# Optimization experiments

Measured on AMD Instinct MI355X. Metric: run time of the kernel, lower is better.

## Reference

```python
import jax, jax.numpy as jnp
import numpy as np

N_SRC0, N_DST0 = 100000, 20000   # block0: 100k src -> 20k dst
N_DST1 = 4096                    # block1: 20k src -> 4096 dst (seed nodes)


def setup_inputs() -> dict:
    key = jax.random.key(0)
    ks = jax.random.split(key, 8)
    E0, E1 = 640000, 131072
    return {
        "features": jax.random.normal(ks[0], (N_SRC0, 256), jnp.float32),
        "W1": jax.random.normal(ks[1], (256, 256), jnp.float32) * (1.0 / np.sqrt(256)),
        "b1": jnp.zeros((256,), jnp.float32),
        "W2": jax.random.normal(ks[2], (256, 128), jnp.float32) * (1.0 / np.sqrt(256)),
        "b2": jnp.zeros((128,), jnp.float32),
        "src0": jax.random.randint(ks[3], (E0,), 0, N_SRC0, jnp.int32),
        "dst0": jax.random.randint(ks[4], (E0,), 0, N_DST0, jnp.int32),
        "src1": jax.random.randint(ks[5], (E1,), 0, N_DST0, jnp.int32),
        "dst1": jax.random.randint(ks[6], (E1,), 0, N_DST1, jnp.int32),
    }


def _graph_conv(src, dst, n_dst, feat, W, b):
    # DGL GraphConv, norm='both': D_out^{-1/2} gather-sum D_in^{-1/2}, then WX+b.
    n_src = feat.shape[0]
    ones = jnp.ones(src.shape[0], feat.dtype)
    out_deg = jax.ops.segment_sum(ones, src, num_segments=n_src)
    norm_src = jnp.clip(out_deg, 1.0, None) ** -0.5          # [n_src]
    h = feat * norm_src[:, None]
    agg = jax.ops.segment_sum(h[src], dst, num_segments=n_dst)  # sparse SpMM
    in_deg = jax.ops.segment_sum(ones, dst, num_segments=n_dst)
    norm_dst = jnp.clip(in_deg, 1.0, None) ** -0.5           # [n_dst]
    return (agg * norm_dst[:, None]) @ W + b


def reference(features, W1, b1, W2, b2, src0, dst0, src1, dst1):
    x = jax.nn.relu(_graph_conv(src0, dst0, N_DST0, features, W1, b1))
    x = _graph_conv(src1, dst1, N_DST1, x, W2, b2)
    return x
```

## Files before the change

kernel.cpp:

```cpp
#include <hip/hip_runtime.h>
#include <hip/hip_bf16.h>

#define K_DIM 256
#define RSTRIDE 128
#define EPB 8192

#define G0_DB 625
#define G0_SB 256
#define G0_SW 392
#define G0_DCAP 48
#define G0_SCAP 80
#define G1_DB 128
#define G1_SB 64
#define G1_SW 313
#define G1_DCAP 128
#define G1_SCAP 224

typedef short bf16x8 __attribute__((ext_vector_type(8)));
typedef float f32x4 __attribute__((ext_vector_type(4)));

static __device__ __forceinline__ unsigned short f2bf(float x) {
    __hip_bfloat16 b = __float2bfloat16(x);
    return *reinterpret_cast<unsigned short*>(&b);
}
static __device__ __forceinline__ float bflo(unsigned int p) {
    return __uint_as_float(p << 16);
}
static __device__ __forceinline__ float bfhi(unsigned int p) {
    return __uint_as_float(p & 0xffff0000u);
}

template <int NDB, int NSB, int SW, int DCAP, int SCP>
static __device__ __forceinline__ void split_graph_sp(
        const int* __restrict__ src, const int* __restrict__ dst, int E, int chunk,
        int* __restrict__ gdcnt, int* __restrict__ gscnt,
        unsigned int* __restrict__ bdst, unsigned int* __restrict__ bsrc,
        int* sh) {
    const int tid = threadIdx.x;
    const int e0 = chunk * EPB;
    const int n = min(EPB, E - e0);
    for (int i = tid; i < NDB + NSB; i += 256) sh[i] = 0;
    __syncthreads();
    for (int j = tid; j < n; j += 256) {
        int d = dst[e0 + j];
        int s = src[e0 + j];
        int bD = d >> 5;
        int rD = atomicAdd(&sh[bD], 1);
        if (rD < DCAP) bdst[((size_t)chunk * NDB + bD) * DCAP + rD] =
            ((unsigned)s << 5) | (unsigned)(d & 31);
        int bS = (int)((unsigned)s / SW);
        int rS = atomicAdd(&sh[NDB + bS], 1);
        if (rS < SCP) bsrc[((size_t)chunk * NSB + bS) * SCP + rS] = (unsigned)s;
    }
    __syncthreads();
    for (int i = tid; i < NDB; i += 256) gdcnt[chunk * NDB + i] = min(sh[i], DCAP);
    for (int i = tid; i < NSB; i += 256) gscnt[chunk * NSB + i] = min(sh[NDB + i], SCP);
}

__global__ __launch_bounds__(256) void split_mega_kernel(
        const int* __restrict__ src0, const int* __restrict__ dst0, int E0,
        const int* __restrict__ src1, const int* __restrict__ dst1, int E1,
        int* __restrict__ gdcnt0, int* __restrict__ gscnt0,
        unsigned int* __restrict__ bdst0, unsigned int* __restrict__ bsrc0,
        int* __restrict__ gdcnt1, int* __restrict__ gscnt1,
        unsigned int* __restrict__ bdst1, unsigned int* __restrict__ bsrc1,
        int nA0, int nA1,
        const float* __restrict__ feat, unsigned short* __restrict__ h, int total_f,
        int castBlocks,
        const float* __restrict__ W1, uint4* __restrict__ pw1,
        const float* __restrict__ W2, uint4* __restrict__ pw2) {
    __shared__ int sh[G0_DB + G0_SB];
    const int b = blockIdx.x;
    if (b < nA0) {
        split_graph_sp<G0_DB, G0_SB, G0_SW, G0_DCAP, G0_SCAP>(
            src0, dst0, E0, b, gdcnt0, gscnt0, bdst0, bsrc0, sh);
    } else if (b < nA0 + nA1) {
        split_graph_sp<G1_DB, G1_SB, G1_SW, G1_DCAP, G1_SCAP>(
            src1, dst1, E1, b - nA0, gdcnt1, gscnt1, bdst1, bsrc1, sh);
    } else if (b < nA0 + nA1 + castBlocks) {
        int idx = ((b - nA0 - nA1) * blockDim.x + threadIdx.x) * 8;
        if (idx >= total_f) return;
        const float4 v0 = *reinterpret_cast<const float4*>(feat + idx);
        const float4 v1 = *reinterpret_cast<const float4*>(feat + idx + 4);
        union { ushort4 u4[2]; uint4 u; } o;
        o.u4[0].x = f2bf(v0.x); o.u4[0].y = f2bf(v0.y);
        o.u4[0].z = f2bf(v0.z); o.u4[0].w = f2bf(v0.w);
        o.u4[1].x = f2bf(v1.x); o.u4[1].y = f2bf(v1.y);
        o.u4[1].z = f2bf(v1.z); o.u4[1].w = f2bf(v1.w);
        *reinterpret_cast<uint4*>(h + idx) = o.u;
    } else if (b < nA0 + nA1 + castBlocks + 32) {
        int idx = (b - nA0 - nA1 - castBlocks) * blockDim.x + threadIdx.x;
        int lane = idx & 63;
        int kt = (idx >> 6) & 7;
        int nt = idx >> 9;
        int n = nt * 16 + (lane & 15);
        int k = kt * 32 + (lane >> 4) * 8;
        union { unsigned short us[8]; uint4 u; } o;
#pragma unroll
        for (int j = 0; j < 8; ++j) o.us[j] = f2bf(W1[(size_t)(k + j) * 256 + n]);
        pw1[idx] = o.u;
    } else {
        int idx = (b - nA0 - nA1 - castBlocks - 32) * blockDim.x + threadIdx.x;
        int lane = idx & 63;
        int kt = (idx >> 6) & 7;
        int nt = idx >> 9;
        int n = nt * 16 + (lane & 15);
        int k = kt * 32 + (lane >> 4) * 8;
        union { unsigned short us[8]; uint4 u; } o;
#pragma unroll
        for (int j = 0; j < 8; ++j) o.us[j] = f2bf(W2[(size_t)(k + j) * 128 + n]);
        pw2[idx] = o.u;
    }
}

__global__ __launch_bounds__(256) void finalize_kernel(
        int nA0, int nA1,
        const unsigned int* __restrict__ bdst0, const int* __restrict__ gdcnt0,
        int* __restrict__ cnt0, int* __restrict__ esrc0,
        const unsigned int* __restrict__ bdst1, const int* __restrict__ gdcnt1,
        int* __restrict__ cnt1, int* __restrict__ esrc1,
        const unsigned int* __restrict__ bsrc0, const int* __restrict__ gscnt0,
        int* __restrict__ od0,
        const unsigned int* __restrict__ bsrc1, const int* __restrict__ gscnt1,
        int* __restrict__ od1) {
    __shared__ int sh[G0_SW];
    const int tid = threadIdx.x;
    int b = blockIdx.x;
    if (b < G0_DB + G1_DB) {
        const bool g0 = b < G0_DB;
        if (!g0) b -= G0_DB;
        const unsigned int* __restrict__ bd = g0 ? bdst0 : bdst1;
        const int* __restrict__ gc = g0 ? gdcnt0 : gdcnt1;
        const int NDB = g0 ? G0_DB : G1_DB;
        const int DCAP = g0 ? G0_DCAP : G1_DCAP;
        const int nblk = g0 ? nA0 : nA1;
        int* __restrict__ esrc = g0 ? esrc0 : esrc1;
        int* __restrict__ cnt = g0 ? cnt0 : cnt1;
        if (tid < 32) sh[tid] = 0;
        __syncthreads();
        for (int rr = (tid >> 2); rr < nblk; rr += 64) {
            const int c = gc[rr * NDB + b];
            const unsigned int* __restrict__ seg = bd + ((size_t)rr * NDB + b) * DCAP;
            for (int j = (tid & 3); j < c; j += 4) {
                unsigned v = seg[j];
                int dloc = v & 31;
                int s = (int)(v >> 5);
                int slot = atomicAdd(&sh[dloc], 1);
                if (slot < RSTRIDE) esrc[((size_t)(b * 32 + dloc) << 7) + slot] = s;
            }
        }
        __syncthreads();
        if (tid < 32) cnt[b * 32 + tid] = sh[tid];
    } else {
        b -= G0_DB + G1_DB;
        const bool g0 = b < G0_SB;
        if (!g0) b -= G0_SB;
        const unsigned int* __restrict__ bs = g0 ? bsrc0 : bsrc1;
        const int* __restrict__ gc = g0 ? gscnt0 : gscnt1;
        const int NSB = g0 ? G0_SB : G1_SB;
        const int SCP = g0 ? G0_SCAP : G1_SCAP;
        const int SW = g0 ? G0_SW : G1_SW;
        const int NN = g0 ? 100000 : 20000;
        const int nblk = g0 ? nA0 : nA1;
        int* __restrict__ od = g0 ? od0 : od1;
        for (int i = tid; i < SW; i += 256) sh[i] = 0;
        __syncthreads();
        const int base = b * SW;
        for (int rr = (tid >> 2); rr < nblk; rr += 64) {
            const int c = gc[rr * NSB + b];
            const unsigned int* __restrict__ seg = bs + ((size_t)rr * NSB + b) * SCP;
            for (int j = (tid & 3); j < c; j += 4)
                atomicAdd(&sh[(int)seg[j] - base], 1);
        }
        __syncthreads();
        for (int i = tid; i < SW; i += 256) {
            int node = base + i;
            if (node < NN) od[node] = sh[i];
        }
    }
}

template <bool NORM>
static __device__ __forceinline__ void gather4_to_lds(
        const unsigned short* __restrict__ hfeat, const int* __restrict__ esrc,
        const int* __restrict__ cnt, const int* __restrict__ od,
        int m0, int w, int lane, unsigned short (*Alds)[264]) {
#pragma unroll
    for (int k = 0; k < 4; ++k) {
        const int rloc = w * 4 + k;
        const int row = m0 + rloc;
        const int c = cnt[row];
        const int cend = min(c, RSTRIDE);
        const int* __restrict__ ep = esrc + ((size_t)row << 7);
        float a0 = 0.f, a1 = 0.f, a2 = 0.f, a3 = 0.f;
        int i = 0;
        for (; i + 3 < cend; i += 4) {
            int s0 = ep[i];
            int s1 = ep[i + 1];
            int s2 = ep[i + 2];
            int s3 = ep[i + 3];
            float n0 = NORM ? rsqrtf((float)max(od[s0], 1)) : 1.0f;
            float n1 = NORM ? rsqrtf((float)max(od[s1], 1)) : 1.0f;
            float n2 = NORM ? rsqrtf((float)max(od[s2], 1)) : 1.0f;
            float n3 = NORM ? rsqrtf((float)max(od[s3], 1)) : 1.0f;
            const uint2 p0 = *reinterpret_cast<const uint2*>(hfeat + (((size_t)s0) << 8) + lane * 4);
            const uint2 p1 = *reinterpret_cast<const uint2*>(hfeat + (((size_t)s1) << 8) + lane * 4);
            const uint2 p2 = *reinterpret_cast<const uint2*>(hfeat + (((size_t)s2) << 8) + lane * 4);
            const uint2 p3 = *reinterpret_cast<const uint2*>(hfeat + (((size_t)s3) << 8) + lane * 4);
            if (NORM) {
                a0 = fmaf(bflo(p0.x), n0, a0); a1 = fmaf(bfhi(p0.x), n0, a1);
                a2 = fmaf(bflo(p0.y), n0, a2); a3 = fmaf(bfhi(p0.y), n0, a3);
                a0 = fmaf(bflo(p1.x), n1, a0); a1 = fmaf(bfhi(p1.x), n1, a1);
                a2 = fmaf(bflo(p1.y), n1, a2); a3 = fmaf(bfhi(p1.y), n1, a3);
                a0 = fmaf(bflo(p2.x), n2, a0); a1 = fmaf(bfhi(p2.x), n2, a1);
                a2 = fmaf(bflo(p2.y), n2, a2); a3 = fmaf(bfhi(p2.y), n2, a3);
                a0 = fmaf(bflo(p3.x), n3, a0); a1 = fmaf(bfhi(p3.x), n3, a1);
                a2 = fmaf(bflo(p3.y), n3, a2); a3 = fmaf(bfhi(p3.y), n3, a3);
            } else {
                a0 += (bflo(p0.x) + bflo(p1.x)) + (bflo(p2.x) + bflo(p3.x));
                a1 += (bfhi(p0.x) + bfhi(p1.x)) + (bfhi(p2.x) + bfhi(p3.x));
                a2 += (bflo(p0.y) + bflo(p1.y)) + (bflo(p2.y) + bflo(p3.y));
                a3 += (bfhi(p0.y) + bfhi(p1.y)) + (bfhi(p2.y) + bfhi(p3.y));
            }
        }
        for (; i < cend; ++i) {
            int s0 = ep[i];
            float n0 = NORM ? rsqrtf((float)max(od[s0], 1)) : 1.0f;
            const uint2 p0 = *reinterpret_cast<const uint2*>(hfeat + (((size_t)s0) << 8) + lane * 4);
            if (NORM) {
                a0 = fmaf(bflo(p0.x), n0, a0); a1 = fmaf(bfhi(p0.x), n0, a1);
                a2 = fmaf(bflo(p0.y), n0, a2); a3 = fmaf(bfhi(p0.y), n0, a3);
            } else {
                a0 += bflo(p0.x);
                a1 += bfhi(p0.x);
                a2 += bflo(p0.y);
                a3 += bfhi(p0.y);
            }
        }
        float nd = rsqrtf((float)max(c, 1));
        ushort4 o;
        o.x = f2bf(a0 * nd);
        o.y = f2bf(a1 * nd);
        o.z = f2bf(a2 * nd);
        o.w = f2bf(a3 * nd);
        *reinterpret_cast<ushort4*>(&Alds[rloc][lane * 4]) = o;
    }
}

__global__ __launch_bounds__(256) void fused0_kernel(
        const unsigned short* __restrict__ hfeat, const int* __restrict__ esrc,
        const int* __restrict__ cnt, const int* __restrict__ od0,
        const uint4* __restrict__ pW, const float* __restrict__ bias,
        const int* __restrict__ od1, unsigned short* __restrict__ out) {
    __shared__ unsigned short Alds[16][264];
    const int m0 = blockIdx.x * 16;
    const int w = threadIdx.x >> 6;
    const int lane = threadIdx.x & 63;
    gather4_to_lds<true>(hfeat, esrc, cnt, od0, m0, w, lane, Alds);
    __syncthreads();

    bf16x8 a[8];
    const unsigned short* ap = &Alds[lane & 15][(lane >> 4) * 8];
#pragma unroll
    for (int kt = 0; kt < 8; ++kt)
        a[kt] = *reinterpret_cast<const bf16x8*>(ap + kt * 32);

    const int rbase = m0 + (lane >> 4) * 4;
    float nsv[4];
#pragma unroll
    for (int r = 0; r < 4; ++r) nsv[r] = rsqrtf((float)max(od1[rbase + r], 1));

#pragma unroll
    for (int nt = 0; nt < 4; ++nt) {
        const int n0 = w * 64 + nt * 16;
        f32x4 acc = {0.f, 0.f, 0.f, 0.f};
#pragma unroll
        for (int kt = 0; kt < 8; ++kt) {
            bf16x8 b = *reinterpret_cast<const bf16x8*>(&pW[((size_t)(n0 >> 4) * 8 + kt) * 64 + lane]);
            acc = __builtin_amdgcn_mfma_f32_16x16x32_bf16(a[kt], b, acc, 0, 0, 0);
        }
        const int col = n0 + (lane & 15);
        const float bv = bias[col];
#pragma unroll
        for (int r = 0; r < 4; ++r) {
            float v = fmaxf(acc[r] + bv, 0.0f) * nsv[r];
            out[(size_t)(rbase + r) * K_DIM + col] = f2bf(v);
        }
    }
}

__global__ __launch_bounds__(256) void fused1_kernel(
        const unsigned short* __restrict__ xb, const int* __restrict__ esrc,
        const int* __restrict__ cnt,
        const uint4* __restrict__ pW, const float* __restrict__ bias,
        float* __restrict__ out) {
    __shared__ unsigned short Alds[16][264];
    const int m0 = blockIdx.x * 16;
    const int w = threadIdx.x >> 6;
    const int lane = threadIdx.x & 63;
    gather4_to_lds<false>(xb, esrc, cnt, nullptr, m0, w, lane, Alds);
    __syncthreads();

    bf16x8 a[8];
    const unsigned short* ap = &Alds[lane & 15][(lane >> 4) * 8];
#pragma unroll
    for (int kt = 0; kt < 8; ++kt)
        a[kt] = *reinterpret_cast<const bf16x8*>(ap + kt * 32);

    const int rbase = m0 + (lane >> 4) * 4;
#pragma unroll
    for (int nt = 0; nt < 2; ++nt) {
        const int n0 = w * 32 + nt * 16;
        f32x4 acc = {0.f, 0.f, 0.f, 0.f};
#pragma unroll
        for (int kt = 0; kt < 8; ++kt) {
            bf16x8 b = *reinterpret_cast<const bf16x8*>(&pW[((size_t)(n0 >> 4) * 8 + kt) * 64 + lane]);
            acc = __builtin_amdgcn_mfma_f32_16x16x32_bf16(a[kt], b, acc, 0, 0, 0);
        }
        const int col = n0 + (lane & 15);
        const float bv = bias[col];
#pragma unroll
        for (int r = 0; r < 4; ++r)
            out[(size_t)(rbase + r) * 128 + col] = acc[r] + bv;
    }
}

__global__ __launch_bounds__(256) void gatherf_kernel(
        const float* __restrict__ feat, const int* __restrict__ esrc,
        const int* __restrict__ cnt, const int* __restrict__ od,
        float* __restrict__ outbuf, int n_dst) {
    int row = blockIdx.x * (blockDim.x >> 6) + (threadIdx.x >> 6);
    int lane = threadIdx.x & 63;
    if (row >= n_dst) return;
    const int c = cnt[row];
    const int cend = min(c, RSTRIDE);
    const int* __restrict__ ep = esrc + ((size_t)row << 7);
    float4 acc = {0.f, 0.f, 0.f, 0.f};
    for (int i = 0; i < cend; ++i) {
        int s0 = ep[i];
        float n0 = rsqrtf((float)max(od[s0], 1));
        const float4 v0 = *reinterpret_cast<const float4*>(feat + (((size_t)s0) << 8) + lane * 4);
        acc.x = fmaf(v0.x, n0, acc.x); acc.y = fmaf(v0.y, n0, acc.y);
        acc.z = fmaf(v0.z, n0, acc.z); acc.w = fmaf(v0.w, n0, acc.w);
    }
    float nd = rsqrtf((float)max(c, 1));
    float4 o = {acc.x * nd, acc.y * nd, acc.z * nd, acc.w * nd};
    *reinterpret_cast<float4*>(outbuf + (((size_t)row) << 8) + lane * 4) = o;
}

__global__ void edges_kernel(const int* __restrict__ src0, const int* __restrict__ dst0,
                             int* __restrict__ od0, int* __restrict__ cnt0,
                             int* __restrict__ esrc0, int E0,
                             const int* __restrict__ src1, const int* __restrict__ dst1,
                             int* __restrict__ od1, int* __restrict__ cnt1,
                             int* __restrict__ esrc1, int E1) {
    int i = blockIdx.x * blockDim.x + threadIdx.x;
    if (i < E0) {
        int s = src0[i];
        int d = dst0[i];
        atomicAdd(&od0[s], 1);
        int slot = atomicAdd(&cnt0[d], 1);
        if (slot < RSTRIDE) esrc0[(d << 7) + slot] = s;
    } else if (i < E0 + E1) {
        int e = i - E0;
        int s = src1[e];
        int d = dst1[e];
        atomicAdd(&od1[s], 1);
        int slot = atomicAdd(&cnt1[d], 1);
        if (slot < RSTRIDE) esrc1[(d << 7) + slot] = s;
    }
}

template <int ROWS, int NCOLS, bool RELU>
__global__ __launch_bounds__(NCOLS) void gemm_kernel(
        const float* __restrict__ A, const float* __restrict__ W,
        const float* __restrict__ bias, float* __restrict__ out, int M) {
    const int row0 = blockIdx.x * ROWS;
    const int c = threadIdx.x;
    const float* __restrict__ Ablk = A + (size_t)row0 * K_DIM;
    const float* __restrict__ Wc = W + c;

    float acc[ROWS];
#pragma unroll
    for (int r = 0; r < ROWS; ++r) acc[r] = 0.0f;

    float w0 = Wc[0];
    float w1 = Wc[NCOLS];
    float w2 = Wc[2 * NCOLS];
    float w3 = Wc[3 * NCOLS];

#pragma unroll 2
    for (int k = 0; k < K_DIM - 4; k += 4) {
        const float* p = Wc + (size_t)(k + 4) * NCOLS;
        float n0 = p[0];
        float n1 = p[NCOLS];
        float n2 = p[2 * NCOLS];
        float n3 = p[3 * NCOLS];
#pragma unroll
        for (int r = 0; r < ROWS; ++r) {
            const float4 a = *reinterpret_cast<const float4*>(Ablk + r * K_DIM + k);
            acc[r] = fmaf(a.x, w0, acc[r]);
            acc[r] = fmaf(a.y, w1, acc[r]);
            acc[r] = fmaf(a.z, w2, acc[r]);
            acc[r] = fmaf(a.w, w3, acc[r]);
        }
        w0 = n0; w1 = n1; w2 = n2; w3 = n3;
    }
    {
        const int k = K_DIM - 4;
#pragma unroll
        for (int r = 0; r < ROWS; ++r) {
            const float4 a = *reinterpret_cast<const float4*>(Ablk + r * K_DIM + k);
            acc[r] = fmaf(a.x, w0, acc[r]);
            acc[r] = fmaf(a.y, w1, acc[r]);
            acc[r] = fmaf(a.z, w2, acc[r]);
            acc[r] = fmaf(a.w, w3, acc[r]);
        }
    }

    const float b = bias[c];
#pragma unroll
    for (int r = 0; r < ROWS; ++r) {
        float v = acc[r] + b;
        if (RELU) v = fmaxf(v, 0.0f);
        out[(size_t)(row0 + r) * NCOLS + c] = v;
    }
}

extern "C" void kernel_launch(void* const* d_in, const int* in_sizes, int n_in,
                              void* d_out, int out_size, void* d_ws, size_t ws_size,
                              hipStream_t stream) {
    const float* features = (const float*)d_in[0];
    const float* W1 = (const float*)d_in[1];
    const float* b1 = (const float*)d_in[2];
    const float* W2 = (const float*)d_in[3];
    const float* b2 = (const float*)d_in[4];
    const int* src0 = (const int*)d_in[5];
    const int* dst0 = (const int*)d_in[6];
    const int* src1 = (const int*)d_in[7];
    const int* dst1 = (const int*)d_in[8];
    const int E0 = in_sizes[5];
    const int E1 = in_sizes[7];
    const int NSRC0 = 100000, NDST0 = 20000, NDST1 = 4096;
    const int nA0 = (E0 + EPB - 1) / EPB;
    const int nA1 = (E1 + EPB - 1) / EPB;

    char* ws = (char*)d_ws;
    size_t off = 0;
    auto carve = [&](size_t bytes) -> void* {
        void* p = ws + off;
        off = (off + bytes + 255) & ~(size_t)255;
        return p;
    };
    int* od0  = (int*)carve((size_t)NSRC0 * 4);
    int* od1  = (int*)carve((size_t)NDST0 * 4);
    int* cnt0 = (int*)carve((size_t)NDST0 * 4);
    int* cnt1 = (int*)carve((size_t)NDST1 * 4);
    const size_t zero_span = off;
    int* esrc0p = (int*)carve((size_t)NDST0 * RSTRIDE * 4);
    int* esrc1p = (int*)carve((size_t)NDST1 * RSTRIDE * 4);
    uint4* pW1  = (uint4*)carve((size_t)8192 * 16);
    uint4* pW2  = (uint4*)carve((size_t)4096 * 16);
    int* gdcnt0 = (int*)carve((size_t)nA0 * G0_DB * 4);
    int* gscnt0 = (int*)carve((size_t)nA0 * G0_SB * 4);
    int* gdcnt1 = (int*)carve((size_t)nA1 * G1_DB * 4);
    int* gscnt1 = (int*)carve((size_t)nA1 * G1_SB * 4);
    unsigned int* bdst0 = (unsigned int*)carve((size_t)nA0 * G0_DB * G0_DCAP * 4);
    unsigned int* bsrc0 = (unsigned int*)carve((size_t)nA0 * G0_SB * G0_SCAP * 4);
    unsigned int* bdst1 = (unsigned int*)carve((size_t)nA1 * G1_DB * G1_DCAP * 4);
    unsigned int* bsrc1 = (unsigned int*)carve((size_t)nA1 * G1_SB * G1_SCAP * 4);
    const size_t region_span = (size_t)((ws + off) - (char*)bdst0);
    const size_t xbufb_bytes = (size_t)NDST0 * K_DIM * 2;
    unsigned short* xbufb = (region_span >= xbufb_bytes)
        ? (unsigned short*)bdst0
        : (unsigned short*)carve(xbufb_bytes);
    const size_t hfeat_bytes = (size_t)NSRC0 * K_DIM * 2;
    unsigned short* hfeat = (unsigned short*)carve(hfeat_bytes);
    const size_t need_bf16 = off;
    (void)n_in; (void)out_size;

    if (ws_size >= need_bf16) {
        const int total_f = NSRC0 * K_DIM;
        const int castBlocks = (total_f / 8 + 255) / 256;
        split_mega_kernel<<<nA0 + nA1 + castBlocks + 48, 256, 0, stream>>>(
            src0, dst0, E0, src1, dst1, E1,
            gdcnt0, gscnt0, bdst0, bsrc0,
            gdcnt1, gscnt1, bdst1, bsrc1,
            nA0, nA1, features, hfeat, total_f, castBlocks,
            W1, pW1, W2, pW2);
        finalize_kernel<<<G0_DB + G1_DB + G0_SB + G1_SB, 256, 0, stream>>>(
            nA0, nA1,
            bdst0, gdcnt0, cnt0, esrc0p,
            bdst1, gdcnt1, cnt1, esrc1p,
            bsrc0, gscnt0, od0,
            bsrc1, gscnt1, od1);
        fused0_kernel<<<NDST0 / 16, 256, 0, stream>>>(
            hfeat, esrc0p, cnt0, od0, pW1, b1, od1, xbufb);
        fused1_kernel<<<NDST1 / 16, 256, 0, stream>>>(
            xbufb, esrc1p, cnt1, pW2, b2, (float*)d_out);
    } else {
        hipMemsetAsync(ws, 0, zero_span, stream);
        float* agg0 = (float*)carve((size_t)NDST0 * K_DIM * 4);
        float* xbuf = (float*)carve((size_t)NDST0 * K_DIM * 4);
        float* agg1 = (float*)carve((size_t)NDST1 * K_DIM * 4);
        edges_kernel<<<(E0 + E1 + 255) / 256, 256, 0, stream>>>(
            src0, dst0, od0, cnt0, esrc0p, E0,
            src1, dst1, od1, cnt1, esrc1p, E1);
        gatherf_kernel<<<(NDST0 + 3) / 4, 256, 0, stream>>>(features, esrc0p, cnt0, od0,
                                                            agg0, NDST0);
        gemm_kernel<16, 256, true><<<NDST0 / 16, 256, 0, stream>>>(agg0, W1, b1, xbuf, NDST0);
        gatherf_kernel<<<(NDST1 + 3) / 4, 256, 0, stream>>>(xbuf, esrc1p, cnt1, od1,
                                                            agg1, NDST1);
        gemm_kernel<4, 128, false><<<NDST1 / 4, 128, 0, stream>>>(agg1, W2, b2,
                                                                  (float*)d_out, NDST1);
    }
}
```

Before: 318.2 us.

## Merge four kernel launches into one cooperative persistent kernel with grid syncs

Replaces the four separate launches (split, finalize, layer-0 fused gather+GEMM, layer-1 fused gather+GEMM) with one cooperative kernel that loops over virtual blocks per phase and separates the phases with grid.sync(). A fallback path launches the same phase bodies as four kernels if the cooperative grid would be too small. It also widens the gather unroll from 4 to 8 edges so more independent loads are in flight. This is meant to remove launch gaps and tail idle time between kernels, at the cost of grid barrier overhead, fewer resident blocks per phase, and higher register pressure.

Measured after the change: 538.9 us. 69.4% more time.

```diff
diff --git a/kernel.cpp b/kernel.cpp
--- a/kernel.cpp
+++ b/kernel.cpp
@@ -1,5 +1,8 @@
 #include <hip/hip_runtime.h>
 #include <hip/hip_bf16.h>
+#include <hip/hip_cooperative_groups.h>
+
+namespace cg = cooperative_groups;
 
 #define K_DIM 256
 #define RSTRIDE 128
@@ -16,8 +19,25 @@
 #define G1_DCAP 128
 #define G1_SCAP 224
 
+#define NB_B (G0_DB + G1_DB + G0_SB + G1_SB)
+#define NB_C 1250
+#define NB_D 256
+
 typedef short bf16x8 __attribute__((ext_vector_type(8)));
 typedef float f32x4 __attribute__((ext_vector_type(4)));
+
+struct GParams {
+    const int* src0; const int* dst0; int E0; int nA0;
+    const int* src1; const int* dst1; int E1; int nA1;
+    int castBlocks; int total_f;
+    const float* feat; unsigned short* hfeat;
+    const float* W1; const float* b1; const float* W2; const float* b2;
+    uint4* pW1; uint4* pW2;
+    int* gdcnt0; int* gscnt0; unsigned int* bdst0; unsigned int* bsrc0;
+    int* gdcnt1; int* gscnt1; unsigned int* bdst1; unsigned int* bsrc1;
+    int* cnt0; int* esrc0; int* cnt1; int* esrc1; int* od0; int* od1;
+    unsigned short* xbufb; float* outp;
+};
 
 static __device__ __forceinline__ unsigned short f2bf(float x) {
     __hip_bfloat16 b = __float2bfloat16(x);
@@ -55,41 +75,31 @@
     __syncthreads();
     for (int i = tid; i < NDB; i += 256) gdcnt[chunk * NDB + i] = min(sh[i], DCAP);
     for (int i = tid; i < NSB; i += 256) gscnt[chunk * NSB + i] = min(sh[NDB + i], SCP);
-}
-
-__global__ __launch_bounds__(256) void split_mega_kernel(
-        const int* __restrict__ src0, const int* __restrict__ dst0, int E0,
-        const int* __restrict__ src1, const int* __restrict__ dst1, int E1,
-        int* __restrict__ gdcnt0, int* __restrict__ gscnt0,
-        unsigned int* __restrict__ bdst0, unsigned int* __restrict__ bsrc0,
-        int* __restrict__ gdcnt1, int* __restrict__ gscnt1,
-        unsigned int* __restrict__ bdst1, unsigned int* __restrict__ bsrc1,
-        int nA0, int nA1,
-        const float* __restrict__ feat, unsigned short* __restrict__ h, int total_f,
-        int castBlocks,
-        const float* __restrict__ W1, uint4* __restrict__ pw1,
-        const float* __restrict__ W2, uint4* __restrict__ pw2) {
-    __shared__ int sh[G0_DB + G0_SB];
-    const int b = blockIdx.x;
-    if (b < nA0) {
+    __syncthreads();
+}
+
+static __device__ __forceinline__ void phaseA_job(int vb, const GParams& P, int* sh) {
+    const int tid = threadIdx.x;
+    if (vb < P.nA0) {
         split_graph_sp<G0_DB, G0_SB, G0_SW, G0_DCAP, G0_SCAP>(
-            src0, dst0, E0, b, gdcnt0, gscnt0, bdst0, bsrc0, sh);
-    } else if (b < nA0 + nA1) {
+            P.src0, P.dst0, P.E0, vb, P.gdcnt0, P.gscnt0, P.bdst0, P.bsrc0, sh);
+    } else if (vb < P.nA0 + P.nA1) {
         split_graph_sp<G1_DB, G1_SB, G1_SW, G1_DCAP, G1_SCAP>(
-            src1, dst1, E1, b - nA0, gdcnt1, gscnt1, bdst1, bsrc1, sh);
-    } else if (b < nA0 + nA1 + castBlocks) {
-        int idx = ((b - nA0 - nA1) * blockDim.x + threadIdx.x) * 8;
-        if (idx >= total_f) return;
-        const float4 v0 = *reinterpret_cast<const float4*>(feat + idx);
-        const float4 v1 = *reinterpret_cast<const float4*>(feat + idx + 4);
-        union { ushort4 u4[2]; uint4 u; } o;
-        o.u4[0].x = f2bf(v0.x); o.u4[0].y = f2bf(v0.y);
-        o.u4[0].z = f2bf(v0.z); o.u4[0].w = f2bf(v0.w);
-        o.u4[1].x = f2bf(v1.x); o.u4[1].y = f2bf(v1.y);
-        o.u4[1].z = f2bf(v1.z); o.u4[1].w = f2bf(v1.w);
-        *reinterpret_cast<uint4*>(h + idx) = o.u;
-    } else if (b < nA0 + nA1 + castBlocks + 32) {
-        int idx = (b - nA0 - nA1 - castBlocks) * blockDim.x + threadIdx.x;
+            P.src1, P.dst1, P.E1, vb - P.nA0, P.gdcnt1, P.gscnt1, P.bdst1, P.bsrc1, sh);
+    } else if (vb < P.nA0 + P.nA1 + P.castBlocks) {
+        int idx = ((vb - P.nA0 - P.nA1) * 256 + tid) * 8;
+        if (idx < P.total_f) {
+            const float4 v0 = *reinterpret_cast<const float4*>(P.feat + idx);
+            const float4 v1 = *reinterpret_cast<const float4*>(P.feat + idx + 4);
+            union { ushort4 u4[2]; uint4 u; } o;
+            o.u4[0].x = f2bf(v0.x); o.u4[0].y = f2bf(v0.y);
+            o.u4[0].z = f2bf(v0.z); o.u4[0].w = f2bf(v0.w);
+            o.u4[1].x = f2bf(v1.x); o.u4[1].y = f2bf(v1.y);
+            o.u4[1].z = f2bf(v1.z); o.u4[1].w = f2bf(v1.w);
+            *reinterpret_cast<uint4*>(P.hfeat + idx) = o.u;
+        }
+    } else if (vb < P.nA0 + P.nA1 + P.castBlocks + 32) {
+        int idx = (vb - P.nA0 - P.nA1 - P.castBlocks) * 256 + tid;
         int lane = idx & 63;
         int kt = (idx >> 6) & 7;
         int nt = idx >> 9;
@@ -97,10 +107,10 @@
         int k = kt * 32 + (lane >> 4) * 8;
         union { unsigned short us[8]; uint4 u; } o;
 #pragma unroll
-        for (int j = 0; j < 8; ++j) o.us[j] = f2bf(W1[(size_t)(k + j) * 256 + n]);
-        pw1[idx] = o.u;
+        for (int j = 0; j < 8; ++j) o.us[j] = f2bf(P.W1[(size_t)(k + j) * 256 + n]);
+        P.pW1[idx] = o.u;
     } else {
-        int idx = (b - nA0 - nA1 - castBlocks - 32) * blockDim.x + threadIdx.x;
+        int idx = (vb - P.nA0 - P.nA1 - P.castBlocks - 32) * 256 + tid;
         int lane = idx & 63;
         int kt = (idx >> 6) & 7;
         int nt = idx >> 9;
@@ -108,34 +118,23 @@
         int k = kt * 32 + (lane >> 4) * 8;
         union { unsigned short us[8]; uint4 u; } o;
 #pragma unroll
-        for (int j = 0; j < 8; ++j) o.us[j] = f2bf(W2[(size_t)(k + j) * 128 + n]);
-        pw2[idx] = o.u;
-    }
-}
-
-__global__ __launch_bounds__(256) void finalize_kernel(
-        int nA0, int nA1,
-        const unsigned int* __restrict__ bdst0, const int* __restrict__ gdcnt0,
-        int* __restrict__ cnt0, int* __restrict__ esrc0,
-        const unsigned int* __restrict__ bdst1, const int* __restrict__ gdcnt1,
-        int* __restrict__ cnt1, int* __restrict__ esrc1,
-        const unsigned int* __restrict__ bsrc0, const int* __restrict__ gscnt0,
-        int* __restrict__ od0,
-        const unsigned int* __restrict__ bsrc1, const int* __restrict__ gscnt1,
-        int* __restrict__ od1) {
-    __shared__ int sh[G0_SW];
+        for (int j = 0; j < 8; ++j) o.us[j] = f2bf(P.W2[(size_t)(k + j) * 128 + n]);
+        P.pW2[idx] = o.u;
+    }
+}
+
+static __device__ __forceinline__ void phaseB_job(int b, const GParams& P, int* sh) {
     const int tid = threadIdx.x;
-    int b = blockIdx.x;
     if (b < G0_DB + G1_DB) {
         const bool g0 = b < G0_DB;
         if (!g0) b -= G0_DB;
-        const unsigned int* __restrict__ bd = g0 ? bdst0 : bdst1;
-        const int* __restrict__ gc = g0 ? gdcnt0 : gdcnt1;
+        const unsigned int* __restrict__ bd = g0 ? P.bdst0 : P.bdst1;
+        const int* __restrict__ gc = g0 ? P.gdcnt0 : P.gdcnt1;
         const int NDB = g0 ? G0_DB : G1_DB;
         const int DCAP = g0 ? G0_DCAP : G1_DCAP;
-        const int nblk = g0 ? nA0 : nA1;
-        int* __restrict__ esrc = g0 ? esrc0 : esrc1;
-        int* __restrict__ cnt = g0 ? cnt0 : cnt1;
+        const int nblk = g0 ? P.nA0 : P.nA1;
+        int* __restrict__ esrc = g0 ? P.esrc0 : P.esrc1;
+        int* __restrict__ cnt = g0 ? P.cnt0 : P.cnt1;
         if (tid < 32) sh[tid] = 0;
         __syncthreads();
         for (int rr = (tid >> 2); rr < nblk; rr += 64) {
@@ -151,18 +150,19 @@
         }
         __syncthreads();
         if (tid < 32) cnt[b * 32 + tid] = sh[tid];
+        __syncthreads();
     } else {
         b -= G0_DB + G1_DB;
         const bool g0 = b < G0_SB;
         if (!g0) b -= G0_SB;
-        const unsigned int* __restrict__ bs = g0 ? bsrc0 : bsrc1;
-        const int* __restrict__ gc = g0 ? gscnt0 : gscnt1;
+        const unsigned int* __restrict__ bs = g0 ? P.bsrc0 : P.bsrc1;
+        const int* __restrict__ gc = g0 ? P.gscnt0 : P.gscnt1;
         const int NSB = g0 ? G0_SB : G1_SB;
         const int SCP = g0 ? G0_SCAP : G1_SCAP;
         const int SW = g0 ? G0_SW : G1_SW;
         const int NN = g0 ? 100000 : 20000;
-        const int nblk = g0 ? nA0 : nA1;
-        int* __restrict__ od = g0 ? od0 : od1;
+        const int nblk = g0 ? P.nA0 : P.nA1;
+        int* __restrict__ od = g0 ? P.od0 : P.od1;
         for (int i = tid; i < SW; i += 256) sh[i] = 0;
         __syncthreads();
         const int base = b * SW;
@@ -177,6 +177,7 @@
             int node = base + i;
             if (node < NN) od[node] = sh[i];
         }
+        __syncthreads();
     }
 }
 
@@ -194,33 +195,50 @@
         const int* __restrict__ ep = esrc + ((size_t)row << 7);
         float a0 = 0.f, a1 = 0.f, a2 = 0.f, a3 = 0.f;
         int i = 0;
+        for (; i + 7 < cend; i += 8) {
+            int s[8];
+            uint2 p[8];
+            float nn[8];
+#pragma unroll
+            for (int u = 0; u < 8; ++u) s[u] = ep[i + u];
+#pragma unroll
+            for (int u = 0; u < 8; ++u)
+                p[u] = *reinterpret_cast<const uint2*>(hfeat + (((size_t)s[u]) << 8) + lane * 4);
+#pragma unroll
+            for (int u = 0; u < 8; ++u)
+                nn[u] = NORM ? rsqrtf((float)max(od[s[u]], 1)) : 1.0f;
+#pragma unroll
+            for (int u = 0; u < 8; ++u) {
+                if (NORM) {
+                    a0 = fmaf(bflo(p[u].x), nn[u], a0); a1 = fmaf(bfhi(p[u].x), nn[u], a1);
+                    a2 = fmaf(bflo(p[u].y), nn[u], a2); a3 = fmaf(bfhi(p[u].y), nn[u], a3);
+                } else {
+                    a0 += bflo(p[u].x); a1 += bfhi(p[u].x);
+                    a2 += bflo(p[u].y); a3 += bfhi(p[u].y);
+                }
+            }
+        }
         for (; i + 3 < cend; i += 4) {
-            int s0 = ep[i];
-            int s1 = ep[i + 1];
-            int s2 = ep[i + 2];
-            int s3 = ep[i + 3];
-            float n0 = NORM ? rsqrtf((float)max(od[s0], 1)) : 1.0f;
-            float n1 = NORM ? rsqrtf((float)max(od[s1], 1)) : 1.0f;
-            float n2 = NORM ? rsqrtf((float)max(od[s2], 1)) : 1.0f;
-            float n3 = NORM ? rsqrtf((float)max(od[s3], 1)) : 1.0f;
-            const uint2 p0 = *reinterpret_cast<const uint2*>(hfeat + (((size_t)s0) << 8) + lane * 4);
-            const uint2 p1 = *reinterpret_cast<const uint2*>(hfeat + (((size_t)s1) << 8) + lane * 4);
-            const uint2 p2 = *reinterpret_cast<const uint2*>(hfeat + (((size_t)s2) << 8) + lane * 4);
-            const uint2 p3 = *reinterpret_cast<const uint2*>(hfeat + (((size_t)s3) << 8) + lane * 4);
-            if (NORM) {
-                a0 = fmaf(bflo(p0.x), n0, a0); a1 = fmaf(bfhi(p0.x), n0, a1);
-                a2 = fmaf(bflo(p0.y), n0, a2); a3 = fmaf(bfhi(p0.y), n0, a3);
-                a0 = fmaf(bflo(p1.x), n1, a0); a1 = fmaf(bfhi(p1.x), n1, a1);
-                a2 = fmaf(bflo(p1.y), n1, a2); a3 = fmaf(bfhi(p1.y), n1, a3);
-                a0 = fmaf(bflo(p2.x), n2, a0); a1 = fmaf(bfhi(p2.x), n2, a1);
-                a2 = fmaf(bflo(p2.y), n2, a2); a3 = fmaf(bfhi(p2.y), n2, a3);
-                a0 = fmaf(bflo(p3.x), n3, a0); a1 = fmaf(bfhi(p3.x), n3, a1);
-                a2 = fmaf(bflo(p3.y), n3, a2); a3 = fmaf(bfhi(p3.y), n3, a3);
-            } else {
-                a0 += (bflo(p0.x) + bflo(p1.x)) + (bflo(p2.x) + bflo(p3.x));
-                a1 += (bfhi(p0.x) + bfhi(p1.x)) + (bfhi(p2.x) + bfhi(p3.x));
-                a2 += (bflo(p0.y) + bflo(p1.y)) + (bflo(p2.y) + bflo(p3.y));
-                a3 += (bfhi(p0.y) + bfhi(p1.y)) + (bfhi(p2.y) + bfhi(p3.y));
+            int s[4];
+            uint2 p[4];
+            float nn[4];
+#pragma unroll
+            for (int u = 0; u < 4; ++u) s[u] = ep[i + u];
+#pragma unroll
+            for (int u = 0; u < 4; ++u)
+                p[u] = *reinterpret_cast<const uint2*>(hfeat + (((size_t)s[u]) << 8) + lane * 4);
+#pragma unroll
+            for (int u = 0; u < 4; ++u)
+                nn[u] = NORM ? rsqrtf((float)max(od[s[u]], 1)) : 1.0f;
+#pragma unroll
+            for (int u = 0; u < 4; ++u) {
+                if (NORM) {
+                    a0 = fmaf(bflo(p[u].x), nn[u], a0); a1 = fmaf(bfhi(p[u].x), nn[u], a1);
+                    a2 = fmaf(bflo(p[u].y), nn[u], a2); a3 = fmaf(bfhi(p[u].y), nn[u], a3);
+                } else {
+                    a0 += bflo(p[u].x); a1 += bfhi(p[u].x);
+                    a2 += bflo(p[u].y); a3 += bfhi(p[u].y);
+                }
             }
         }
         for (; i < cend; ++i) {
@@ -231,10 +249,8 @@
                 a0 = fmaf(bflo(p0.x), n0, a0); a1 = fmaf(bfhi(p0.x), n0, a1);
                 a2 = fmaf(bflo(p0.y), n0, a2); a3 = fmaf(bfhi(p0.y), n0, a3);
             } else {
-                a0 += bflo(p0.x);
-                a1 += bfhi(p0.x);
-                a2 += bflo(p0.y);
-                a3 += bfhi(p0.y);
+                a0 += bflo(p0.x); a1 += bfhi(p0.x);
+                a2 += bflo(p0.y); a3 += bfhi(p0.y);
             }
         }
         float nd = rsqrtf((float)max(c, 1));
@@ -247,16 +263,12 @@
     }
 }
 
-__global__ __launch_bounds__(256) void fused0_kernel(
-        const unsigned short* __restrict__ hfeat, const int* __restrict__ esrc,
-        const int* __restrict__ cnt, const int* __restrict__ od0,
-        const uint4* __restrict__ pW, const float* __restrict__ bias,
-        const int* __restrict__ od1, unsigned short* __restrict__ out) {
-    __shared__ unsigned short Alds[16][264];
-    const int m0 = blockIdx.x * 16;
+static __device__ __forceinline__ void fused0_tile(
+        int t, const GParams& P, unsigned short (*Alds)[264]) {
+    const int m0 = t * 16;
     const int w = threadIdx.x >> 6;
     const int lane = threadIdx.x & 63;
-    gather4_to_lds<true>(hfeat, esrc, cnt, od0, m0, w, lane, Alds);
+    gather4_to_lds<true>(P.hfeat, P.esrc0, P.cnt0, P.od0, m0, w, lane, Alds);
     __syncthreads();
 
     bf16x8 a[8];
@@ -268,7 +280,7 @@
     const int rbase = m0 + (lane >> 4) * 4;
     float nsv[4];
 #pragma unroll
-    for (int r = 0; r < 4; ++r) nsv[r] = rsqrtf((float)max(od1[rbase + r], 1));
+    for (int r = 0; r < 4; ++r) nsv[r] = rsqrtf((float)max(P.od1[rbase + r], 1));
 
 #pragma unroll
     for (int nt = 0; nt < 4; ++nt) {
@@ -276,29 +288,26 @@
         f32x4 acc = {0.f, 0.f, 0.f, 0.f};
 #pragma unroll
         for (int kt = 0; kt < 8; ++kt) {
-            bf16x8 b = *reinterpret_cast<const bf16x8*>(&pW[((size_t)(n0 >> 4) * 8 + kt) * 64 + lane]);
+            bf16x8 b = *reinterpret_cast<const bf16x8*>(&P.pW1[((size_t)(n0 >> 4) * 8 + kt) * 64 + lane]);
             acc = __builtin_amdgcn_mfma_f32_16x16x32_bf16(a[kt], b, acc, 0, 0, 0);
         }
         const int col = n0 + (lane & 15);
-        const float bv = bias[col];
+        const float bv = P.b1[col];
 #pragma unroll
         for (int r = 0; r < 4; ++r) {
             float v = fmaxf(acc[r] + bv, 0.0f) * nsv[r];
-            out[(size_t)(rbase + r) * K_DIM + col] = f2bf(v);
-        }
-    }
-}
-
-__global__ __launch_bounds__(256) void fused1_kernel(
-        const unsigned short* __restrict__ xb, const int* __restrict__ esrc,
-        const int* __restrict__ cnt,
-        const uint4* __restrict__ pW, const float* __restrict__ bias,
-        float* __restrict__ out) {
-    __shared__ unsigned short Alds[16][264];
-    const int m0 = blockIdx.x * 16;
+            P.xbufb[(size_t)(rbase + r) * K_DIM + col] = f2bf(v);
+        }
+    }
+    __syncthreads();
+}
+
+static __device__ __forceinline__ void fused1_tile(
+        int t, const GParams& P, unsigned short (*Alds)[264]) {
+    const int m0 = t * 16;
     const int w = threadIdx.x >> 6;
     const int lane = threadIdx.x & 63;
-    gather4_to_lds<false>(xb, esrc, cnt, nullptr, m0, w, lane, Alds);
+    gather4_to_lds<false>(P.xbufb, P.esrc1, P.cnt1, nullptr, m0, w, lane, Alds);
     __syncthreads();
 
     bf16x8 a[8];
@@ -314,15 +323,50 @@
         f32x4 acc = {0.f, 0.f, 0.f, 0.f};
 #pragma unroll
         for (int kt = 0; kt < 8; ++kt) {
-            bf16x8 b = *reinterpret_cast<const bf16x8*>(&pW[((size_t)(n0 >> 4) * 8 + kt) * 64 + lane]);
+            bf16x8 b = *reinterpret_cast<const bf16x8*>(&P.pW2[((size_t)(n0 >> 4) * 8 + kt) * 64 + lane]);
             acc = __builtin_amdgcn_mfma_f32_16x16x32_bf16(a[kt], b, acc, 0, 0, 0);
         }
         const int col = n0 + (lane & 15);
-        const float bv = bias[col];
+        const float bv = P.b2[col];
 #pragma unroll
         for (int r = 0; r < 4; ++r)
-            out[(size_t)(rbase + r) * 128 + col] = acc[r] + bv;
-    }
+            P.outp[(size_t)(rbase + r) * 128 + col] = acc[r] + bv;
+    }
+    __syncthreads();
+}
+
+__global__ __launch_bounds__(256, 4) void gcn_coop_kernel(GParams P) {
+    __shared__ alignas(16) char smem[8704];
+    cg::grid_group grid = cg::this_grid();
+    const int totalA = P.nA0 + P.nA1 + P.castBlocks + 48;
+    for (int vb = blockIdx.x; vb < totalA; vb += gridDim.x)
+        phaseA_job(vb, P, (int*)smem);
+    grid.sync();
+    for (int vb = blockIdx.x; vb < NB_B; vb += gridDim.x)
+        phaseB_job(vb, P, (int*)smem);
+    grid.sync();
+    for (int vb = blockIdx.x; vb < NB_C; vb += gridDim.x)
+        fused0_tile(vb, P, (unsigned short (*)[264])smem);
+    grid.sync();
+    for (int vb = blockIdx.x; vb < NB_D; vb += gridDim.x)
+        fused1_tile(vb, P, (unsigned short (*)[264])smem);
+}
+
+__global__ __launch_bounds__(256) void phaseA_kernel(GParams P) {
+    __shared__ alignas(16) int sh[G0_DB + G0_SB];
+    phaseA_job(blockIdx.x, P, sh);
+}
+__global__ __launch_bounds__(256) void phaseB_kernel(GParams P) {
+    __shared__ alignas(16) int sh[G0_SW];
+    phaseB_job(blockIdx.x, P, sh);
+}
+__global__ __launch_bounds__(256) void phaseC_kernel(GParams P) {
+    __shared__ alignas(16) unsigned short Alds[16][264];
+    fused0_tile(blockIdx.x, P, Alds);
+}
+__global__ __launch_bounds__(256) void phaseD_kernel(GParams P) {
+    __shared__ alignas(16) unsigned short Alds[16][264];
+    fused1_tile(blockIdx.x, P, Alds);
 }
 
 __global__ __launch_bounds__(256) void gatherf_kernel(
@@ -482,22 +526,42 @@
     if (ws_size >= need_bf16) {
         const int total_f = NSRC0 * K_DIM;
         const int castBlocks = (total_f / 8 + 255) / 256;
-        split_mega_kernel<<<nA0 + nA1 + castBlocks + 48, 256, 0, stream>>>(
-            src0, dst0, E0, src1, dst1, E1,
-            gdcnt0, gscnt0, bdst0, bsrc0,
-            gdcnt1, gscnt1, bdst1, bsrc1,
-            nA0, nA1, features, hfeat, total_f, castBlocks,
-            W1, pW1, W2, pW2);
-        finalize_kernel<<<G0_DB + G1_DB + G0_SB + G1_SB, 256, 0, stream>>>(
-            nA0, nA1,
-            bdst0, gdcnt0, cnt0, esrc0p,
-            bdst1, gdcnt1, cnt1, esrc1p,
-            bsrc0, gscnt0, od0,
-            bsrc1, gscnt1, od1);
-        fused0_kernel<<<NDST0 / 16, 256, 0, stream>>>(
-            hfeat, esrc0p, cnt0, od0, pW1, b1, od1, xbufb);
-        fused1_kernel<<<NDST1 / 16, 256, 0, stream>>>(
-            xbufb, esrc1p, cnt1, pW2, b2, (float*)d_out);
+
+        GParams prm;
+        prm.src0 = src0; prm.dst0 = dst0; prm.E0 = E0; prm.nA0 = nA0;
+        prm.src1 = src1; prm.dst1 = dst1; prm.E1 = E1; prm.nA1 = nA1;
+        prm.castBlocks = castBlocks; prm.total_f = total_f;
+        prm.feat = features; prm.hfeat = hfeat;
+        prm.W1 = W1; prm.b1 = b1; prm.W2 = W2; prm.b2 = b2;
+        prm.pW1 = pW1; prm.pW2 = pW2;
+        prm.gdcnt0 = gdcnt0; prm.gscnt0 = gscnt0; prm.bdst0 = bdst0; prm.bsrc0 = bsrc0;
+        prm.gdcnt1 = gdcnt1; prm.gscnt1 = gscnt1; prm.bdst1 = bdst1; prm.bsrc1 = bsrc1;
+        prm.cnt0 = cnt0; prm.esrc0 = esrc0p; prm.cnt1 = cnt1; prm.esrc1 = esrc1p;
+        prm.od0 = od0; prm.od1 = od1;
+        prm.xbufb = xbufb; prm.outp = (float*)d_out;
+
+        static int coopBlocks = -1;
+        if (coopBlocks < 0) {
+            int occ = 0, cus = 0, dev = 0;
+            hipGetDevice(&dev);
+            hipDeviceGetAttribute(&cus, hipDeviceAttributeMultiprocessorCount, dev);
+            hipError_t e = hipOccupancyMaxActiveBlocksPerMultiprocessor(
+                &occ, gcn_coop_kernel, 256, 0);
+            coopBlocks = (e == hipSuccess && occ > 0 && cus > 0)
+                             ? min(occ * cus, 2048) : 0;
+        }
+
+        if (coopBlocks >= 256) {
+            void* kargs[] = { (void*)&prm };
+            hipLaunchCooperativeKernel((void*)gcn_coop_kernel, dim3(coopBlocks),
+                                       dim3(256), kargs, 0, stream);
+        } else {
+            const int totalA = nA0 + nA1 + castBlocks + 48;
+            phaseA_kernel<<<totalA, 256, 0, stream>>>(prm);
+            phaseB_kernel<<<NB_B, 256, 0, stream>>>(prm);
+            phaseC_kernel<<<NB_C, 256, 0, stream>>>(prm);
+            phaseD_kernel<<<NB_D, 256, 0, stream>>>(prm);
+        }
     } else {
         hipMemsetAsync(ws, 0, zero_span, stream);
         float* agg0 = (float*)carve((size_t)NDST0 * K_DIM * 4);
```
